# Kernel optimization log

Measured on AMD Instinct MI355X. Metric: run time of the kernel, lower is better.

## Reference

```python
import jax, jax.numpy as jnp
import numpy as np

L_IN, L_FREQ, L_OUT = 128, 64, 64
C_IN, C_OUT, T_DIM = 64, 64, 256
SPIN = 1

# ---------- self-contained spin-weighted SHT (MW sampling), replacing s2fft ----------

def _mw_thetas(L, extended):
    n = 2 * L - 1 if extended else L
    return (2 * np.arange(n) + 1) * np.pi / (2 * L - 1)

def _wigner_d_stack(L, thetas, n):
    # d^l_{m,n}(theta) = <l,m| exp(-i theta Jy) |l,n>, computed via eigh of the
    # Hermitian angular-momentum operator Jy. Output (ntheta, L, 2L-1), m at col L-1+m.
    nth = len(thetas)
    out = np.zeros((nth, L, 2 * L - 1), dtype=np.float64)
    for l in range(abs(n), L):
        dim = 2 * l + 1
        m = np.arange(-l, l).astype(np.float64)
        ap = np.sqrt(l * (l + 1.0) - m * (m + 1.0))
        Jy = np.zeros((dim, dim), dtype=np.complex128)
        i = np.arange(dim - 1)
        Jy[i + 1, i] = -0.5j * ap
        Jy[i, i + 1] = 0.5j * ap
        lam, V = np.linalg.eigh(Jy)
        coeff = V * np.conj(V[l + n, :])[None, :]
        phases = np.exp(-1j * np.outer(lam, thetas))
        out[:, l, L - 1 - l:L + l] = (coeff @ phases).T.real
    return out

def _mw_quad_weights(L):
    # per-theta weights on the mirror-extended grid: q_t = (1/(2L-1)) sum_k w(k) e^{ik theta_t}
    # with w(k) = int_0^pi e^{ik t} sin(t) dt
    k = np.arange(-(L - 1), L)
    den = np.where(np.abs(k) == 1, 1, 1 - k * k).astype(np.float64)
    w = np.where(k % 2 == 0, 2.0 / den, 0.0).astype(np.complex128)
    w[k == 1] = 0.5j * np.pi
    w[k == -1] = -0.5j * np.pi
    th = _mw_thetas(L, True)
    return ((w[None, :] * np.exp(1j * np.outer(th, k))).sum(1) / (2 * L - 1)).real

# transform kernels are constants (built once at import, numpy)
_D_FWD = jnp.asarray(_wigner_d_stack(L_IN, _mw_thetas(L_IN, True), -SPIN) * _mw_quad_weights(L_IN)[:, None, None], jnp.float32)
_D_INV = jnp.asarray(_wigner_d_stack(L_OUT, _mw_thetas(L_OUT, False), -SPIN), jnp.float32)
_CL_IN = jnp.asarray(((-1.0) ** SPIN) * np.sqrt((2 * np.arange(L_IN) + 1) / (4 * np.pi)), jnp.float32)
_CL_OUT = jnp.asarray(((-1.0) ** SPIN) * np.sqrt((2 * np.arange(L_OUT) + 1) / (4 * np.pi)), jnp.float32)
_m_all = np.arange(-(L_IN - 1), L_IN)
_PARITY = jnp.asarray(np.where((_m_all + SPIN) % 2 == 0, 1.0, -1.0), jnp.float32)

def sht_forward(x):
    # x: (L_IN, 2*L_IN-1, C) real spatial -> flm: (L_IN, 2*L_IN-1, C) complex, m at L_IN-1+m
    nphi = 2 * L_IN - 1
    ftm = jnp.fft.fftshift(jnp.fft.fft(x, axis=1), axes=1) * (2 * jnp.pi / nphi)
    # mirror extension in theta with (-1)^(m+spin) parity (all channels at once)
    g_ext = jnp.concatenate([ftm, _PARITY[None, :, None] * ftm[::-1][1:]], axis=0)
    flm = jnp.einsum('tlm,tmc->lmc', _D_FWD, g_ext)
    return flm * _CL_IN[:, None, None]

def sht_inverse(flm):
    # flm: (L_OUT, 2*L_OUT-1, C) complex -> (L_OUT, 2*L_OUT-1, C) real spatial
    ftm = jnp.einsum('tlm,lmc->tmc', _D_INV, flm * _CL_OUT[:, None, None])
    return (jnp.fft.ifft(jnp.fft.ifftshift(ftm, axes=1), axis=1) * (2 * L_OUT - 1)).real

def resize_flm(flm, l_in, l_out):
    # centered truncation / zero-pad of (L, 2L-1, C) harmonic coefficients
    if l_out <= l_in:
        d = l_in - l_out
        return flm[:l_out, d:d + 2 * l_out - 1]
    d = l_out - l_in
    return jnp.pad(flm, ((0, d), (d, d), (0, 0)))

# ---------- inputs and parameters ----------

def setup_inputs():
    key = jax.random.key(0)
    ks = jax.random.split(key, 12)
    n = lambda i, shape, s: jax.random.normal(ks[i], shape, jnp.float32) * s
    return {
        'x': jax.random.normal(ks[0], (L_IN, 2 * L_IN - 1, C_IN), jnp.float32),
        't_emb': jax.random.normal(ks[1], (T_DIM,), jnp.float32),
        'spec_conv_w': n(2, (C_IN, C_OUT), (1.0 / C_IN) ** 0.5),
        'spec_conv_b': jnp.zeros((C_OUT,), jnp.float32),
        'spec_wr': n(3, (L_FREQ, C_IN, C_OUT), (0.5 / C_IN) ** 0.5),
        'spec_wi': n(4, (L_FREQ, C_IN, C_OUT), (0.5 / C_IN) ** 0.5),
        'spec_tr_w': n(5, (T_DIM, L_FREQ), (1.0 / T_DIM) ** 0.5),
        'spec_tr_b': jnp.zeros((L_FREQ,), jnp.float32),
        'spec_ti_w': n(6, (T_DIM, L_FREQ), (1.0 / T_DIM) ** 0.5),
        'spec_ti_b': jnp.zeros((L_FREQ,), jnp.float32),
        'spat_conv1_w': n(7, (C_IN, C_OUT), (1.0 / C_IN) ** 0.5),
        'spat_conv1_b': jnp.zeros((C_OUT,), jnp.float32),
        'spat_t_w': n(8, (T_DIM, 2 * C_OUT), (1.0 / T_DIM) ** 0.5),
        'spat_t_b': jnp.zeros((2 * C_OUT,), jnp.float32),
        'spat_weight': n(9, (C_OUT, C_OUT), 0.01),
        'spat_conv2_w': n(10, (C_OUT, C_OUT), (1.0 / C_OUT) ** 0.5),
        'spat_conv2_b': jnp.zeros((C_OUT,), jnp.float32),
        'ln_scale': jnp.ones((C_OUT,), jnp.float32),
        'ln_bias': jnp.zeros((C_OUT,), jnp.float32),
    }

def reference(x, t_emb, spec_conv_w, spec_conv_b, spec_wr, spec_wi, spec_tr_w, spec_tr_b, spec_ti_w, spec_ti_b, spat_conv1_w, spat_conv1_b, spat_t_w, spat_t_b, spat_weight, spat_conv2_w, spat_conv2_b, ln_scale, ln_bias):
    # ----- SphericalSpectralTimeConv branch -----
    flm = sht_forward(x)                                   # (L_IN, 2L_IN-1, C_IN) complex
    flm = resize_flm(flm, L_IN, L_FREQ)                    # (L_FREQ, 2L_FREQ-1, C_IN)
    conv_flm = jnp.einsum('lmi,io->lmo', flm, spec_conv_w) + spec_conv_b
    t_c = (t_emb @ spec_tr_w + spec_tr_b) + 1j * (t_emb @ spec_ti_w + spec_ti_b)   # (L_FREQ,)
    w = t_c[:, None, None] * (spec_wr + 1j * spec_wi)      # (L_FREQ, C_IN, C_OUT)
    flm = jnp.einsum('lmi,lio->lmo', flm, w) + conv_flm
    xs = sht_inverse(resize_flm(flm, L_FREQ, L_OUT))       # (L_OUT, 2L_OUT-1, C_OUT) real
    xs = xs / (jnp.linalg.norm(xs, axis=-1, keepdims=True) + 1e-6)
    # ----- SpatialTimeConv branch (path='down') -----
    h = jnp.einsum('lmi,io->lmo', x, spat_conv1_w) + spat_conv1_b
    t = t_emb @ spat_t_w + spat_t_b
    w_t, b_t = t[:C_OUT], t[C_OUT:]
    h = jnp.einsum('lmi,io->lmo', h, w_t[None, :] * spat_weight)
    h = sht_inverse(resize_flm(sht_forward(h), L_IN, L_OUT))
    h = jnp.einsum('lmi,io->lmo', h, spat_conv2_w) + spat_conv2_b + b_t
    # ----- combine: add, gelu, LayerNorm (eps=1e-6 over channels) -----
    y = jax.nn.gelu(xs + h)
    mu = jnp.mean(y, axis=-1, keepdims=True)
    var = jnp.var(y, axis=-1, keepdims=True)
    return (y - mu) * jax.lax.rsqrt(var + 1e-6) * ln_scale + ln_bias
```

## Files before the change

### kernel.cpp

```cpp
#include <hip/hip_runtime.h>
#include <math.h>

#define DPI 3.141592653589793238462643383279502884

__device__ float g_Deff[1040384];
__device__ float g_Dinv[520192];
__device__ int g_wig_done = 0;

__device__ __forceinline__ float wave_sum64(float v) {
#pragma unroll
  for (int off = 32; off > 0; off >>= 1) v += __shfl_xor(v, off, 64);
  return v;
}

__device__ __forceinline__ float gelu_tanh(float v) {
  float u = 0.7978845608028654f * (v + 0.044715f * v * v * v);
  return 0.5f * v * (1.0f + tanhf(u));
}

#define CN255F ((float)(-2.0 * DPI / 255.0))
#define CN127F ((float)(2.0 * DPI / 127.0))

__device__ __forceinline__ void dft_block(int idx, int tid, const float* __restrict__ x,
                                          float* __restrict__ Are, float* __restrict__ Aim,
                                          float* __restrict__ Bre, float* __restrict__ Bim,
                                          char* sm) {
  float* xs_ = (float*)sm;
  int t = idx >> 2, ph = (idx >> 1) & 1, mh = idx & 1;
  float* ore = ph ? Bre : Are;
  float* oim = ph ? Bim : Aim;
  int pbase = ph * 128;
  int Ktot = ph ? 127 : 128;
  int cg_ = tid & 15, mg = tid >> 4;
  float wr[2], wi[2], rc[2], rs[2];
#pragma unroll
  for (int j = 0; j < 2; ++j) {
    int m = mh * 32 + mg * 2 + j;
    __sincosf(CN255F * (float)m, &rs[j], &rc[j]);
    int r0 = (m * pbase) % 255;
    __sincosf(CN255F * (float)r0, &wi[j], &wr[j]);
  }
  float accr[2][4], acci[2][4];
#pragma unroll
  for (int j = 0; j < 2; ++j)
#pragma unroll
    for (int q = 0; q < 4; ++q) { accr[j][q] = 0.f; acci[j][q] = 0.f; }
  for (int k0 = 0; k0 < Ktot; k0 += 64) {
    int kn = (Ktot - k0 < 64) ? Ktot - k0 : 64;
    __syncthreads();
    {
      const float4* src = (const float4*)(x + ((size_t)t * 255 + pbase + k0) * 64);
      float4* dst = (float4*)xs_;
      int lim = kn * 16;
#pragma unroll
      for (int q = 0; q < 4; ++q) {
        int fidx = tid + q * 256;
        if (fidx < lim) dst[fidx] = src[fidx];
      }
    }
    __syncthreads();
#pragma unroll 2
    for (int k = 0; k < kn; ++k) {
      float4 xv = *(const float4*)&xs_[k * 64 + cg_ * 4];
      float xv4[4] = {xv.x, xv.y, xv.z, xv.w};
#pragma unroll
      for (int j = 0; j < 2; ++j) {
#pragma unroll
        for (int q = 0; q < 4; ++q) {
          accr[j][q] = fmaf(xv4[q], wr[j], accr[j][q]);
          acci[j][q] = fmaf(xv4[q], wi[j], acci[j][q]);
        }
        float nw = wr[j] * rc[j] - wi[j] * rs[j];
        wi[j] = fmaf(wr[j], rs[j], wi[j] * rc[j]);
        wr[j] = nw;
      }
    }
  }
#pragma unroll
  for (int j = 0; j < 2; ++j) {
    int mi = mh * 32 + mg * 2 + j;
    size_t ob = ((size_t)t * 64 + mi) * 64 + cg_ * 4;
    *(float4*)(ore + ob) = make_float4(accr[j][0], accr[j][1], accr[j][2], accr[j][3]);
    *(float4*)(oim + ob) = make_float4(acci[j][0], acci[j][1], acci[j][2], acci[j][3]);
  }
}

__device__ __forceinline__ void wigner_block(int wb, int tid, char* sm) {
  if (__hip_atomic_load(&g_wig_done, __ATOMIC_RELAXED, __HIP_MEMORY_SCOPE_AGENT)) return;
  float* LF = (float*)sm;
  double* red = (double*)(sm + 512);
  float* clf = (float*)(sm + 1024);
  int mode = (wb < 128) ? 0 : 1;
  int t, mm;
  if (mode == 0) { t = wb; mm = tid; }
  else { mm = wb - 128; t = (tid < 64) ? tid : 63; }
  if (tid < 64) clf[tid] = (float)(-sqrt((2.0 * tid + 1.0) / (4.0 * DPI)));
  if (tid < 128) LF[tid] = (tid == 0) ? 0.f : logf((float)tid);
  __syncthreads();
  for (int s = 1; s < 128; s <<= 1) {
    float add = (tid < 128 && tid >= s) ? LF[tid - s] : 0.f;
    __syncthreads();
    if (tid < 128) LF[tid] += add;
    __syncthreads();
  }
  double denomN = (mode == 0) ? 255.0 : 127.0;
  double beta = (2.0 * t + 1.0) * DPI / denomN;
  float coeff = 1.0f;
  if (mode == 0) {
    if (tid < 63) {
      int k = 2 * (tid + 1);
      red[tid] = 8.0 * cos((double)k * beta) / (1.0 - (double)k * (double)k);
    } else if (tid == 63) {
      red[63] = 4.0;
    }
    __syncthreads();
    for (int s = 32; s > 0; s >>= 1) {
      if (tid < s) red[tid] += red[tid + s];
      __syncthreads();
    }
    double s = red[0] / 255.0;
    if (t == 127) s *= 0.5;
    coeff = (float)(s * (2.0 * DPI / 255.0));
  }
  bool active = (mode == 0) ? (tid < 127) : (tid < 64);
  if (!active) return;
  int m = mm - 63;
  double chd, shd;
  sincos(0.5 * beta, &shd, &chd);
  float cbf = (float)cos(beta);
  float chf = (float)chd, shf = (float)shd;
  int am = (m < 0) ? -m : m;
  int l0v = (am > 1) ? am : 1;
  float seed;
  if (m == 0) {
    seed = -1.4142135623730951f * shf * chf;
  } else {
    int j = am;
    float lch = logf(chf), lsh = logf(shf);
    float e0 = 0.5f * (LF[2 * j] - LF[j - 1] - LF[j + 1]);
    float expo = (m >= 1) ? e0 + (float)(j - 1) * lch + (float)(j + 1) * lsh
                          : e0 + (float)(j + 1) * lch + (float)(j - 1) * lsh;
    float sv = __expf(expo);
    seed = (m >= 1 && ((m + 1) & 1)) ? -sv : sv;
  }
  float dl = seed, dm1 = 0.0f, S_cur = 0.0f;
  float mf = (float)m;
  for (int l = 0; l < 64; ++l) {
    float val = 0.0f;
    if (l >= l0v) {
      val = dl * coeff * clf[l];
      float Ld = (float)l, lp = Ld + 1.0f;
      float S_next = sqrtf((lp * lp - mf * mf) * (lp * lp - 1.0f));
      float num1 = (2.0f * Ld + 1.0f) * (Ld * lp * cbf + mf);
      float dn = (num1 * dl - lp * S_cur * dm1) / (Ld * S_next);
      dm1 = dl; dl = dn; S_cur = S_next;
    }
    if (mode == 0) g_Deff[((size_t)t * 127 + mm) * 64 + l] = val;
    else g_Dinv[((size_t)mm * 64 + l) * 64 + t] = val;
  }
}

__device__ __forceinline__ void a2_block(int l, int tid, const float* __restrict__ temb,
                                         const float* __restrict__ trw, const float* __restrict__ trb,
                                         const float* __restrict__ tiw, const float* __restrict__ tib,
                                         const float* __restrict__ scw, const float* __restrict__ swr,
                                         const float* __restrict__ swi, float2* __restrict__ A2,
                                         char* sm) {
  float* fb1 = (float*)sm;
  float* fb2 = (float*)(sm + 1024);
  fb1[tid] = temb[tid] * trw[tid * 64 + l];
  fb2[tid] = temb[tid] * tiw[tid * 64 + l];
  __syncthreads();
  for (int s = 128; s > 0; s >>= 1) {
    if (tid < s) { fb1[tid] += fb1[tid + s]; fb2[tid] += fb2[tid + s]; }
    __syncthreads();
  }
  float tr = fb1[0] + trb[l], ti = fb2[0] + tib[l];
  int o = tid & 63, iq = tid >> 6;
#pragma unroll 4
  for (int i = iq * 16; i < iq * 16 + 16; ++i) {
    int idx = (l * 64 + i) * 64 + o;
    float r = swr[idx], s2 = swi[idx];
    A2[idx] = make_float2(scw[i * 64 + o] + tr * r - ti * s2, tr * s2 + ti * r);
  }
}

__device__ __forceinline__ void mstv_block(int tid, const float* __restrict__ temb,
                                           const float* __restrict__ stw, const float* __restrict__ stb,
                                           const float* __restrict__ c1w, const float* __restrict__ c1b,
                                           const float* __restrict__ sweight,
                                           float* __restrict__ tv, float* __restrict__ Mm,
                                           float* __restrict__ bias2, char* sm) {
  float* temb_s = (float*)sm;
  float* swt = (float*)(sm + 1024);
  float* c1s = (float*)(sm + 17408);
  float* tvo_s = (float*)(sm + 34048);
  if (tid < 64) ((float4*)temb_s)[tid] = ((const float4*)temb)[tid];
  for (int q = tid; q < 1024; q += 256) ((float4*)swt)[q] = ((const float4*)sweight)[q];
  for (int e = tid; e < 4096; e += 256) c1s[(e >> 6) * 65 + (e & 63)] = c1w[e];
  __syncthreads();
  if (tid < 128) {
    float a0 = 0.f, a1 = 0.f, a2 = 0.f, a3 = 0.f;
#pragma unroll 8
    for (int k = 0; k < 256; k += 4) {
      a0 = fmaf(temb_s[k],     stw[k * 128 + tid],       a0);
      a1 = fmaf(temb_s[k + 1], stw[(k + 1) * 128 + tid], a1);
      a2 = fmaf(temb_s[k + 2], stw[(k + 2) * 128 + tid], a2);
      a3 = fmaf(temb_s[k + 3], stw[(k + 3) * 128 + tid], a3);
    }
    float tvv = a0 + a1 + a2 + a3 + stb[tid];
    tv[tid] = tvv;
    if (tid < 64) tvo_s[tid] = tvv;
  }
  __syncthreads();
  {
    int j = tid >> 2, ob = (tid & 3) * 16;
    float acc[16];
#pragma unroll
    for (int q = 0; q < 16; ++q) acc[q] = 0.f;
    for (int i = 0; i < 64; ++i) {
      float c = c1s[j * 65 + i];
#pragma unroll
      for (int q = 0; q < 16; ++q) acc[q] = fmaf(c, swt[i * 64 + ob + q], acc[q]);
    }
#pragma unroll
    for (int q = 0; q < 16; ++q) Mm[j * 64 + ob + q] = tvo_s[ob + q] * acc[q];
  }
  if (tid < 64) {
    float acc = 0.f;
#pragma unroll 4
    for (int i = 0; i < 64; ++i) acc = fmaf(c1b[i], swt[i * 64 + tid], acc);
    bias2[tid] = tvo_s[tid] * acc;
  }
}

__global__ __launch_bounds__(256, 2) void ct_pre(
    const float* __restrict__ x,
    float* __restrict__ ftmA_re, float* __restrict__ ftmA_im,
    float* __restrict__ ftmB_re, float* __restrict__ ftmB_im) {
  __shared__ __align__(16) char sm[16384];
  int vb = blockIdx.x;
  int tid = threadIdx.x;
  if (vb < 255) wigner_block(vb, tid, sm);
  else dft_block(vb - 255, tid, x, ftmA_re, ftmA_im, ftmB_re, ftmB_im, sm);
}

__global__ __launch_bounds__(256) void ct_projf(const float* __restrict__ fAre,
                                                const float* __restrict__ fAim,
                                                const float* __restrict__ fBre,
                                                const float* __restrict__ fBim,
                                                float* __restrict__ flmA_re, float* __restrict__ flmA_im,
                                                float* __restrict__ flmB_re, float* __restrict__ flmB_im,
                                                const float* __restrict__ temb,
                                                const float* __restrict__ trw, const float* __restrict__ trb,
                                                const float* __restrict__ tiw, const float* __restrict__ tib,
                                                const float* __restrict__ scw, const float* __restrict__ swr,
                                                const float* __restrict__ swi, float2* __restrict__ A2,
                                                const float* __restrict__ stw, const float* __restrict__ stb,
                                                const float* __restrict__ c1w, const float* __restrict__ c1b,
                                                const float* __restrict__ sweight,
                                                float* __restrict__ tv, float* __restrict__ Mm,
                                                float* __restrict__ bias2) {
  __shared__ __align__(16) char sm[40960];
  int tile = blockIdx.x;
  int tid = threadIdx.x;
  if (tile >= 508) {
    if (tile < 572) a2_block(tile - 508, tid, temb, trw, trb, tiw, tib, scw, swr, swi, A2, sm);
    else mstv_block(tid, temb, stw, stb, c1w, c1b, sweight, tv, Mm, bias2, sm);
    return;
  }
  float (*Dsh)[32] = (float(*)[32])(sm);
  float (*fr_)[64] = (float(*)[64])(sm + 8192);
  float (*fi_)[64] = (float(*)[64])(sm + 24576);
  int mm = tile >> 2, lh = (tile >> 1) & 1, th = tile & 1;
  float* ore = th ? flmB_re : flmA_re;
  float* oim = th ? flmB_im : flmA_im;
  int tb = th * 64;
  int mi = (mm >= 63) ? (mm - 63) : (63 - mm);
  float csign = (mm >= 63) ? 1.0f : -1.0f;
  int cg_ = tid & 15, lg = tid >> 4;
  for (int e = tid; e < 64 * 32; e += 256) {
    int r = e >> 5, li = e & 31;
    Dsh[r][li] = g_Deff[((size_t)(tb + r) * 127 + mm) * 64 + lh * 32 + li];
  }
  for (int e = tid; e < 64 * 64; e += 256) {
    int r = e >> 6, c = e & 63;
    size_t idx = ((size_t)(tb + r) * 64 + mi) * 64 + c;
    fr_[r][c] = fAre[idx] + fBre[idx];
    fi_[r][c] = csign * (fAim[idx] + fBim[idx]);
  }
  __syncthreads();
  float ar[2][4], ai[2][4];
#pragma unroll
  for (int li = 0; li < 2; ++li)
#pragma unroll
    for (int q = 0; q < 4; ++q) { ar[li][q] = 0.f; ai[li][q] = 0.f; }
#pragma unroll 4
  for (int k = 0; k < 64; ++k) {
    float4 fr4 = *(const float4*)&fr_[k][cg_ * 4];
    float4 fi4 = *(const float4*)&fi_[k][cg_ * 4];
    float2 d2 = *(const float2*)&Dsh[k][lg * 2];
    float frv[4] = {fr4.x, fr4.y, fr4.z, fr4.w};
    float fiv[4] = {fi4.x, fi4.y, fi4.z, fi4.w};
    float dv[2] = {d2.x, d2.y};
#pragma unroll
    for (int li = 0; li < 2; ++li)
#pragma unroll
      for (int q = 0; q < 4; ++q) {
        ar[li][q] = fmaf(dv[li], frv[q], ar[li][q]);
        ai[li][q] = fmaf(dv[li], fiv[q], ai[li][q]);
      }
  }
#pragma unroll
  for (int li = 0; li < 2; ++li) {
    size_t row = ((size_t)mm * 64 + lh * 32 + lg * 2 + li) * 64 + cg_ * 4;
    *(float4*)(ore + row) = make_float4(ar[li][0], ar[li][1], ar[li][2], ar[li][3]);
    *(float4*)(oim + row) = make_float4(ai[li][0], ai[li][1], ai[li][2], ai[li][3]);
  }
}

__global__ __launch_bounds__(256) void ct_mix(const float* __restrict__ flmA_re,
                                              const float* __restrict__ flmA_im,
                                              const float* __restrict__ flmB_re,
                                              const float* __restrict__ flmB_im,
                                              const float2* __restrict__ A2,
                                              const float* __restrict__ Mm,
                                              const float* __restrict__ scb,
                                              const float* __restrict__ bias2,
                                              float* __restrict__ s_re, float* __restrict__ s_im,
                                              float* __restrict__ h_re, float* __restrict__ h_im) {
  __shared__ float Ar_[64][32], Ai_[64][32], Msh[64][32];
  __shared__ float Br_[64][65], Bi_[64][65];
  __shared__ float rb[256];
  int l = blockIdx.x, mh = blockIdx.y, oh = blockIdx.z;
  int tid = threadIdx.x;
  int og = tid & 15, mg = tid >> 4;
  rb[tid] = (mh == 0 && tid < 128) ? g_Deff[((size_t)tid * 127 + 63) * 64 + l] : 0.f;
  __syncthreads();
  for (int s = 128; s > 0; s >>= 1) {
    if (tid < s) rb[tid] += rb[tid + s];
    __syncthreads();
  }
  float slv = rb[0];
  for (int e = tid; e < 64 * 32; e += 256) {
    int r = e >> 5, oi = e & 31;
    float2 aa = A2[((size_t)l * 64 + r) * 64 + oh * 32 + oi];
    Ar_[r][oi] = aa.x; Ai_[r][oi] = aa.y;
    Msh[r][oi] = Mm[r * 64 + oh * 32 + oi];
  }
  for (int e = tid; e < 64 * 64; e += 256) {
    int mi = e >> 6, i = e & 63;
    int gmm = mh * 64 + mi; if (gmm > 126) gmm = 126;
    size_t idx = ((size_t)gmm * 64 + l) * 64 + i;
    Br_[mi][i] = flmA_re[idx] + flmB_re[idx];
    Bi_[mi][i] = flmA_im[idx] + flmB_im[idx];
  }
  __syncthreads();
  int o0 = oh * 32 + og * 2;
  float b0[2] = {scb[o0], scb[o0 + 1]};
  float sr[4][2], si[4][2], hr[4][2], hi[4][2];
#pragma unroll
  for (int jm = 0; jm < 4; ++jm)
#pragma unroll
    for (int qo = 0; qo < 2; ++qo) {
      sr[jm][qo] = b0[qo]; si[jm][qo] = 0.f; hr[jm][qo] = 0.f; hi[jm][qo] = 0.f;
    }
#pragma unroll 4
  for (int k = 0; k < 64; ++k) {
    float2 ar2 = *(const float2*)&Ar_[k][og * 2];
    float2 ai2 = *(const float2*)&Ai_[k][og * 2];
    float2 mv2 = *(const float2*)&Msh[k][og * 2];
    float br4[4], bi4[4];
#pragma unroll
    for (int jm = 0; jm < 4; ++jm) {
      br4[jm] = Br_[mg * 4 + jm][k];
      bi4[jm] = Bi_[mg * 4 + jm][k];
    }
    float arv[2] = {ar2.x, ar2.y}, aiv[2] = {ai2.x, ai2.y}, mvv[2] = {mv2.x, mv2.y};
#pragma unroll
    for (int jm = 0; jm < 4; ++jm)
#pragma unroll
      for (int qo = 0; qo < 2; ++qo) {
        sr[jm][qo] = fmaf(br4[jm], arv[qo], sr[jm][qo]);
        sr[jm][qo] = fmaf(-bi4[jm], aiv[qo], sr[jm][qo]);
        si[jm][qo] = fmaf(br4[jm], aiv[qo], si[jm][qo]);
        si[jm][qo] = fmaf(bi4[jm], arv[qo], si[jm][qo]);
        hr[jm][qo] = fmaf(br4[jm], mvv[qo], hr[jm][qo]);
        hi[jm][qo] = fmaf(bi4[jm], mvv[qo], hi[jm][qo]);
      }
  }
  float bb[2] = {bias2[o0], bias2[o0 + 1]};
#pragma unroll
  for (int jm = 0; jm < 4; ++jm) {
    int gmm = mh * 64 + mg * 4 + jm;
    if (gmm > 126) continue;
    if (gmm == 63) {
#pragma unroll
      for (int qo = 0; qo < 2; ++qo)
        hr[jm][qo] = fmaf(255.0f * slv, bb[qo], hr[jm][qo]);
    }
    size_t row = ((size_t)gmm * 64 + l) * 64 + o0;
    *(float2*)(s_re + row) = make_float2(sr[jm][0], sr[jm][1]);
    *(float2*)(s_im + row) = make_float2(si[jm][0], si[jm][1]);
    *(float2*)(h_re + row) = make_float2(hr[jm][0], hr[jm][1]);
    *(float2*)(h_im + row) = make_float2(hi[jm][0], hi[jm][1]);
  }
}

__global__ __launch_bounds__(256) void ct_proji(const float* __restrict__ s_re,
                                                const float* __restrict__ s_im,
                                                const float* __restrict__ h_re,
                                                const float* __restrict__ h_im,
                                                float* __restrict__ fos_re, float* __restrict__ fos_im,
                                                float* __restrict__ foh_re, float* __restrict__ foh_im) {
  __shared__ float Dsh[64][64];
  __shared__ float Br_[64][32], Bi_[64][32];
  int mm = blockIdx.x, br = blockIdx.y, ch = blockIdx.z;
  const float* ire = br ? h_re : s_re;
  const float* iim = br ? h_im : s_im;
  float* ore = br ? foh_re : fos_re;
  float* oim = br ? foh_im : fos_im;
  int tid = threadIdx.x;
  int cg_ = tid & 15, tg = tid >> 4;
  for (int e = tid; e < 64 * 64; e += 256) {
    int r = e >> 6, tt = e & 63;
    Dsh[r][tt] = g_Dinv[((size_t)mm * 64 + r) * 64 + tt];
  }
  for (int e = tid; e < 64 * 32; e += 256) {
    int r = e >> 5, cc = e & 31;
    size_t idx = ((size_t)mm * 64 + r) * 64 + ch * 32 + cc;
    Br_[r][cc] = ire[idx];
    Bi_[r][cc] = iim[idx];
  }
  __syncthreads();
  float ar[4][2], ai[4][2];
#pragma unroll
  for (int j = 0; j < 4; ++j)
#pragma unroll
    for (int q = 0; q < 2; ++q) { ar[j][q] = 0.f; ai[j][q] = 0.f; }
#pragma unroll 4
  for (int k = 0; k < 64; ++k) {
    float4 d4 = *(const float4*)&Dsh[k][tg * 4];
    float2 fr2 = *(const float2*)&Br_[k][cg_ * 2];
    float2 fi2 = *(const float2*)&Bi_[k][cg_ * 2];
    float dv[4] = {d4.x, d4.y, d4.z, d4.w};
    float frv[2] = {fr2.x, fr2.y}, fiv[2] = {fi2.x, fi2.y};
#pragma unroll
    for (int j = 0; j < 4; ++j)
#pragma unroll
      for (int q = 0; q < 2; ++q) {
        ar[j][q] = fmaf(dv[j], frv[q], ar[j][q]);
        ai[j][q] = fmaf(dv[j], fiv[q], ai[j][q]);
      }
  }
#pragma unroll
  for (int j = 0; j < 4; ++j) {
    int t = tg * 4 + j;
    size_t ob = ((size_t)t * 127 + mm) * 64 + ch * 32 + cg_ * 2;
    *(float2*)(ore + ob) = make_float2(ar[j][0], ar[j][1]);
    *(float2*)(oim + ob) = make_float2(ai[j][0], ai[j][1]);
  }
}

__global__ __launch_bounds__(256) void ct_idft(const float* __restrict__ fos_re,
                                               const float* __restrict__ fos_im,
                                               const float* __restrict__ foh_re,
                                               const float* __restrict__ foh_im,
                                               float* __restrict__ xsbA, float* __restrict__ xsbB,
                                               float* __restrict__ hsbA, float* __restrict__ hsbB) {
  __shared__ float Br_[32][64], Bi_[32][64];
  int t = blockIdx.x, br = blockIdx.y;
  int z = blockIdx.z;
  int ph = z >> 1, kh = z & 1;
  const float* fre = br ? foh_re : fos_re;
  const float* fim = br ? foh_im : fos_im;
  float* outp = br ? (kh ? hsbB : hsbA) : (kh ? xsbB : xsbA);
  int kbase = kh * 64;
  int Ktot = kh ? 63 : 64;
  int tid = threadIdx.x;
  int cg_ = tid & 15, pg = tid >> 4;
  float wc[4], ws[4], rc[4], rs[4];
#pragma unroll
  for (int j = 0; j < 4; ++j) {
    int gp = ph * 64 + pg * 4 + j; if (gp > 126) gp = 126;
    __sincosf(CN127F * (float)gp, &rs[j], &rc[j]);
    int r0 = ((kbase - 63) * gp) % 127;
    __sincosf(CN127F * (float)r0, &ws[j], &wc[j]);
  }
  float acc[4][4];
#pragma unroll
  for (int j = 0; j < 4; ++j)
#pragma unroll
    for (int q = 0; q < 4; ++q) acc[j][q] = 0.f;
  for (int k0 = 0; k0 < Ktot; k0 += 32) {
    int kn = (Ktot - k0 < 32) ? Ktot - k0 : 32;
    __syncthreads();
    for (int e = tid; e < 32 * 64; e += 256) {
      int r = e >> 6, j = e & 63;
      if (r < kn) {
        size_t bidx = ((size_t)t * 127 + kbase + k0 + r) * 64 + j;
        Br_[r][j] = fre[bidx]; Bi_[r][j] = fim[bidx];
      }
    }
    __syncthreads();
#pragma unroll 2
    for (int k = 0; k < kn; ++k) {
      float4 b_r = *(const float4*)&Br_[k][cg_ * 4];
      float4 b_i = *(const float4*)&Bi_[k][cg_ * 4];
      float brv[4] = {b_r.x, b_r.y, b_r.z, b_r.w};
      float biv[4] = {b_i.x, b_i.y, b_i.z, b_i.w};
#pragma unroll
      for (int j = 0; j < 4; ++j) {
#pragma unroll
        for (int q = 0; q < 4; ++q) {
          acc[j][q] = fmaf(brv[q], wc[j], acc[j][q]);
          acc[j][q] = fmaf(biv[q], -ws[j], acc[j][q]);
        }
        float nw = wc[j] * rc[j] - ws[j] * rs[j];
        ws[j] = fmaf(wc[j], rs[j], ws[j] * rc[j]);
        wc[j] = nw;
      }
    }
  }
#pragma unroll
  for (int j = 0; j < 4; ++j) {
    int gp = ph * 64 + pg * 4 + j;
    if (gp > 126) continue;
    *(float4*)(outp + ((size_t)t * 127 + gp) * 64 + cg_ * 4) =
        make_float4(acc[j][0], acc[j][1], acc[j][2], acc[j][3]);
  }
}

__global__ __launch_bounds__(256) void ct_fin(const float* __restrict__ xsbA,
                                              const float* __restrict__ xsbB,
                                              const float* __restrict__ hsbA,
                                              const float* __restrict__ hsbB,
                                              const float* __restrict__ c2w,
                                              const float* __restrict__ c2b,
                                              const float* __restrict__ tv,
                                              const float* __restrict__ lns,
                                              const float* __restrict__ lnb,
                                              float* __restrict__ out) {
  int w = threadIdx.x >> 6, lane = threadIdx.x & 63;
  size_t row = (size_t)blockIdx.x * 4 + w;
  size_t base = row * 64 + lane;
  float hv = hsbA[base] + hsbB[base];
  float xv = xsbA[base] + xsbB[base];
  float acc = c2b[lane] + tv[64 + lane];
#pragma unroll 16
  for (int i = 0; i < 64; ++i)
    acc = fmaf(__shfl(hv, i, 64), c2w[i * 64 + lane], acc);
  float ss = wave_sum64(xv * xv);
  xv = xv / (sqrtf(ss) + 1e-6f);
  float y = xv + acc;
  float g = gelu_tanh(y);
  float mu = wave_sum64(g) * (1.0f / 64.0f);
  float d = g - mu;
  float var = wave_sum64(d * d) * (1.0f / 64.0f);
  out[base] = d * rsqrtf(var + 1e-6f) * lns[lane] + lnb[lane];
  if (blockIdx.x == 0 && threadIdx.x == 0)
    __hip_atomic_store(&g_wig_done, 1, __ATOMIC_RELAXED, __HIP_MEMORY_SCOPE_AGENT);
}

extern "C" void kernel_launch(void* const* d_in, const int* in_sizes, int n_in,
                              void* d_out, int out_size, void* d_ws, size_t ws_size,
                              hipStream_t stream) {
  const float* x = (const float*)d_in[0];
  const float* temb = (const float*)d_in[1];
  const float* scw = (const float*)d_in[2];
  const float* scb = (const float*)d_in[3];
  const float* swr = (const float*)d_in[4];
  const float* swi = (const float*)d_in[5];
  const float* strw = (const float*)d_in[6];
  const float* strb = (const float*)d_in[7];
  const float* stiw = (const float*)d_in[8];
  const float* stib = (const float*)d_in[9];
  const float* c1w = (const float*)d_in[10];
  const float* c1b = (const float*)d_in[11];
  const float* stw = (const float*)d_in[12];
  const float* stb = (const float*)d_in[13];
  const float* sweight = (const float*)d_in[14];
  const float* c2w = (const float*)d_in[15];
  const float* c2b = (const float*)d_in[16];
  const float* lns = (const float*)d_in[17];
  const float* lnb = (const float*)d_in[18];
  float* out = (float*)d_out;

  char* base = (char*)d_ws;
  size_t off = 0;
  auto alloc = [&](size_t bytes) -> void* {
    void* p = base + off;
    off += (bytes + 255) & ~(size_t)255;
    return p;
  };
  float* tv = (float*)alloc(128 * sizeof(float));
  float* Mm = (float*)alloc(4096 * sizeof(float));
  float* bias2 = (float*)alloc(64 * sizeof(float));
  float2* A2 = (float2*)alloc(262144 * sizeof(float2));
  float* fosbuf = (float*)alloc(1040384 * sizeof(float));
  float* ftmA_re = (float*)alloc(524288 * sizeof(float));
  float* ftmA_im = (float*)alloc(524288 * sizeof(float));
  float* ftmB_re = (float*)alloc(524288 * sizeof(float));
  float* ftmB_im = (float*)alloc(524288 * sizeof(float));
  float* flmA_re = (float*)alloc(520192 * sizeof(float));
  float* flmA_im = (float*)alloc(520192 * sizeof(float));
  float* flmB_re = (float*)alloc(520192 * sizeof(float));
  float* flmB_im = (float*)alloc(520192 * sizeof(float));
  if (off > ws_size) return;
  float* s_re = ftmA_re;
  float* s_im = ftmA_im;
  float* h_re = ftmB_re;
  float* h_im = ftmB_im;
  float* fos_re = fosbuf;
  float* fos_im = fosbuf + 520192;
  float* foh_re = flmA_re;
  float* foh_im = flmA_im;
  float* xsbA = flmB_re;
  float* xsbB = flmB_im;
  float* hsbA = ftmA_re;
  float* hsbB = ftmA_im;

  hipLaunchKernelGGL(ct_pre, dim3(767), dim3(256), 0, stream,
                     x, ftmA_re, ftmA_im, ftmB_re, ftmB_im);
  hipLaunchKernelGGL(ct_projf, dim3(573), dim3(256), 0, stream,
                     ftmA_re, ftmA_im, ftmB_re, ftmB_im,
                     flmA_re, flmA_im, flmB_re, flmB_im,
                     temb, strw, strb, stiw, stib, scw, swr, swi, A2,
                     stw, stb, c1w, c1b, sweight, tv, Mm, bias2);
  hipLaunchKernelGGL(ct_mix, dim3(64, 2, 2), dim3(256), 0, stream,
                     flmA_re, flmA_im, flmB_re, flmB_im, A2, Mm, scb, bias2,
                     s_re, s_im, h_re, h_im);
  hipLaunchKernelGGL(ct_proji, dim3(127, 2, 2), dim3(256), 0, stream,
                     s_re, s_im, h_re, h_im, fos_re, fos_im, foh_re, foh_im);
  hipLaunchKernelGGL(ct_idft, dim3(64, 2, 4), dim3(256), 0, stream,
                     fos_re, fos_im, foh_re, foh_im, xsbA, xsbB, hsbA, hsbB);
  hipLaunchKernelGGL(ct_fin, dim3(2032), dim3(256), 0, stream, xsbA, xsbB, hsbA, hsbB,
                     c2w, c2b, tv, lns, lnb, out);
}
```

Before: 179.0 us.

## Fuse forward projection, spectral mix and inverse projection into one per-m kernel

The forward Wigner projection, the channel mixing and the inverse Wigner projection are merged into a single ct_mid kernel with one block per (m, output-half). Intermediate flm and mixed spectra stay in shared memory instead of going through global buffers. The A2 and Mm/bias precomputation moves into ct_pre, leaving four launches instead of six. The trade-off is only 254 blocks, heavier per-block work and large shared memory use. The forward projection is also computed twice, once for each output half.

Result: no change. 182.2 us (+1.8%).

```diff
diff --git a/kernel.cpp b/kernel.cpp
--- a/kernel.cpp
+++ b/kernel.cpp
@@ -235,230 +235,182 @@
 }
 
 __global__ __launch_bounds__(256, 2) void ct_pre(
-    const float* __restrict__ x,
+    const float* __restrict__ x, const float* __restrict__ temb,
+    const float* __restrict__ trw, const float* __restrict__ trb,
+    const float* __restrict__ tiw, const float* __restrict__ tib,
+    const float* __restrict__ stw, const float* __restrict__ stb,
+    const float* __restrict__ scw, const float* __restrict__ swr,
+    const float* __restrict__ swi, const float* __restrict__ c1w,
+    const float* __restrict__ c1b, const float* __restrict__ sweight,
+    float2* __restrict__ A2, float* __restrict__ Mm,
+    float* __restrict__ bias2, float* __restrict__ tv,
     float* __restrict__ ftmA_re, float* __restrict__ ftmA_im,
     float* __restrict__ ftmB_re, float* __restrict__ ftmB_im) {
-  __shared__ __align__(16) char sm[16384];
+  __shared__ __align__(16) char sm[34304];
   int vb = blockIdx.x;
   int tid = threadIdx.x;
   if (vb < 255) wigner_block(vb, tid, sm);
-  else dft_block(vb - 255, tid, x, ftmA_re, ftmA_im, ftmB_re, ftmB_im, sm);
-}
-
-__global__ __launch_bounds__(256) void ct_projf(const float* __restrict__ fAre,
-                                                const float* __restrict__ fAim,
-                                                const float* __restrict__ fBre,
-                                                const float* __restrict__ fBim,
-                                                float* __restrict__ flmA_re, float* __restrict__ flmA_im,
-                                                float* __restrict__ flmB_re, float* __restrict__ flmB_im,
-                                                const float* __restrict__ temb,
-                                                const float* __restrict__ trw, const float* __restrict__ trb,
-                                                const float* __restrict__ tiw, const float* __restrict__ tib,
-                                                const float* __restrict__ scw, const float* __restrict__ swr,
-                                                const float* __restrict__ swi, float2* __restrict__ A2,
-                                                const float* __restrict__ stw, const float* __restrict__ stb,
-                                                const float* __restrict__ c1w, const float* __restrict__ c1b,
-                                                const float* __restrict__ sweight,
-                                                float* __restrict__ tv, float* __restrict__ Mm,
-                                                float* __restrict__ bias2) {
-  __shared__ __align__(16) char sm[40960];
-  int tile = blockIdx.x;
+  else if (vb < 767) dft_block(vb - 255, tid, x, ftmA_re, ftmA_im, ftmB_re, ftmB_im, sm);
+  else if (vb < 831) a2_block(vb - 767, tid, temb, trw, trb, tiw, tib, scw, swr, swi, A2, sm);
+  else mstv_block(tid, temb, stw, stb, c1w, c1b, sweight, tv, Mm, bias2, sm);
+}
+
+__global__ __launch_bounds__(256, 2) void ct_mid(
+    const float* __restrict__ fAre, const float* __restrict__ fAim,
+    const float* __restrict__ fBre, const float* __restrict__ fBim,
+    const float2* __restrict__ A2, const float* __restrict__ Mm,
+    const float* __restrict__ scb, const float* __restrict__ bias2,
+    float* __restrict__ fos_re, float* __restrict__ fos_im,
+    float* __restrict__ foh_re, float* __restrict__ foh_im) {
+  __shared__ __align__(16) char sm[69888];
+  int mm = blockIdx.x, oh = blockIdx.y;
   int tid = threadIdx.x;
-  if (tile >= 508) {
-    if (tile < 572) a2_block(tile - 508, tid, temb, trw, trb, tiw, tib, scw, swr, swi, A2, sm);
-    else mstv_block(tid, temb, stw, stb, c1w, c1b, sweight, tv, Mm, bias2, sm);
-    return;
-  }
-  float (*Dsh)[32] = (float(*)[32])(sm);
-  float (*fr_)[64] = (float(*)[64])(sm + 8192);
-  float (*fi_)[64] = (float(*)[64])(sm + 24576);
-  int mm = tile >> 2, lh = (tile >> 1) & 1, th = tile & 1;
-  float* ore = th ? flmB_re : flmA_re;
-  float* oim = th ? flmB_im : flmA_im;
-  int tb = th * 64;
   int mi = (mm >= 63) ? (mm - 63) : (63 - mm);
   float csign = (mm >= 63) ? 1.0f : -1.0f;
-  int cg_ = tid & 15, lg = tid >> 4;
-  for (int e = tid; e < 64 * 32; e += 256) {
-    int r = e >> 5, li = e & 31;
-    Dsh[r][li] = g_Deff[((size_t)(tb + r) * 127 + mm) * 64 + lh * 32 + li];
-  }
-  for (int e = tid; e < 64 * 64; e += 256) {
-    int r = e >> 6, c = e & 63;
-    size_t idx = ((size_t)(tb + r) * 64 + mi) * 64 + c;
-    fr_[r][c] = fAre[idx] + fBre[idx];
-    fi_[r][c] = csign * (fAim[idx] + fBim[idx]);
-  }
-  __syncthreads();
-  float ar[2][4], ai[2][4];
-#pragma unroll
-  for (int li = 0; li < 2; ++li)
+
+  float* flm_re = (float*)(sm);
+  float* flm_im = (float*)(sm + 17408);
+  float* sS_re  = (float*)(sm + 34816);
+  float* sS_im  = (float*)(sm + 43520);
+  float* hS_re  = (float*)(sm + 52224);
+  float* hS_im  = (float*)(sm + 60928);
+  float* slS    = (float*)(sm + 69632);
+  float* fre_s = (float*)(sm + 34816);
+  float* fim_s = (float*)(sm + 43008);
+  float* Dt    = (float*)(sm + 51200);
+  float* Dsh = (float*)(sm);
+
+  int cg = tid & 15, lg = tid >> 4;
+  float ar[4][4], ai[4][4], sl4[4];
+#pragma unroll
+  for (int li = 0; li < 4; ++li) {
+    sl4[li] = 0.f;
 #pragma unroll
     for (int q = 0; q < 4; ++q) { ar[li][q] = 0.f; ai[li][q] = 0.f; }
+  }
+  for (int t0 = 0; t0 < 128; t0 += 32) {
+    __syncthreads();
+    for (int e = tid; e < 2048; e += 256) {
+      int r = e >> 6, c = e & 63;
+      size_t idx = ((size_t)(t0 + r) * 64 + mi) * 64 + c;
+      fre_s[r * 64 + c] = fAre[idx] + fBre[idx];
+      fim_s[r * 64 + c] = csign * (fAim[idx] + fBim[idx]);
+      Dt[r * 64 + c] = g_Deff[((size_t)(t0 + r) * 127 + mm) * 64 + c];
+    }
+    __syncthreads();
+#pragma unroll 2
+    for (int k = 0; k < 32; ++k) {
+      float4 fr4 = *(const float4*)&fre_s[k * 64 + cg * 4];
+      float4 fi4 = *(const float4*)&fim_s[k * 64 + cg * 4];
+      float4 d4 = *(const float4*)&Dt[k * 64 + lg * 4];
+      float frv[4] = {fr4.x, fr4.y, fr4.z, fr4.w};
+      float fiv[4] = {fi4.x, fi4.y, fi4.z, fi4.w};
+      float dv[4] = {d4.x, d4.y, d4.z, d4.w};
+#pragma unroll
+      for (int li = 0; li < 4; ++li) {
+        sl4[li] += dv[li];
+#pragma unroll
+        for (int q = 0; q < 4; ++q) {
+          ar[li][q] = fmaf(dv[li], frv[q], ar[li][q]);
+          ai[li][q] = fmaf(dv[li], fiv[q], ai[li][q]);
+        }
+      }
+    }
+  }
+  __syncthreads();
+#pragma unroll
+  for (int li = 0; li < 4; ++li) {
+    int l = lg * 4 + li;
+    *(float4*)&flm_re[l * 68 + cg * 4] = make_float4(ar[li][0], ar[li][1], ar[li][2], ar[li][3]);
+    *(float4*)&flm_im[l * 68 + cg * 4] = make_float4(ai[li][0], ai[li][1], ai[li][2], ai[li][3]);
+    if (cg == 0) slS[l] = sl4[li];
+  }
+  __syncthreads();
+
+  {
+    int lB = tid >> 2;
+    int oq = tid & 3;
+    int o0 = oh * 32 + oq * 8;
+    float sr[8], si2[8], hr[8], hi2[8];
+#pragma unroll
+    for (int q = 0; q < 8; ++q) {
+      sr[q] = scb[o0 + q]; si2[q] = 0.f; hr[q] = 0.f; hi2[q] = 0.f;
+    }
+    for (int i = 0; i < 64; ++i) {
+      float fr = flm_re[lB * 68 + i];
+      float fi = flm_im[lB * 68 + i];
+      const float2* a2p = &A2[((size_t)lB * 64 + i) * 64 + o0];
+      const float* mmp = &Mm[i * 64 + o0];
+#pragma unroll
+      for (int q = 0; q < 8; ++q) {
+        float2 a = a2p[q];
+        float mv = mmp[q];
+        sr[q] = fmaf(fr, a.x, fmaf(-fi, a.y, sr[q]));
+        si2[q] = fmaf(fr, a.y, fmaf(fi, a.x, si2[q]));
+        hr[q] = fmaf(fr, mv, hr[q]);
+        hi2[q] = fmaf(fi, mv, hi2[q]);
+      }
+    }
+    if (mm == 63) {
+      float sl = 255.0f * slS[lB];
+#pragma unroll
+      for (int q = 0; q < 8; ++q) hr[q] = fmaf(sl, bias2[o0 + q], hr[q]);
+    }
+    int ob = oq * 8;
+#pragma unroll
+    for (int q = 0; q < 8; ++q) {
+      sS_re[lB * 34 + ob + q] = sr[q];
+      sS_im[lB * 34 + ob + q] = si2[q];
+      hS_re[lB * 34 + ob + q] = hr[q];
+      hS_im[lB * 34 + ob + q] = hi2[q];
+    }
+  }
+  __syncthreads();
+
+  for (int e = tid; e < 4096; e += 256) {
+    int r = e >> 6, tt = e & 63;
+    Dsh[r * 64 + tt] = g_Dinv[((size_t)mm * 64 + r) * 64 + tt];
+  }
+  __syncthreads();
+  {
+    int cg2 = tid & 15, tg = tid >> 4;
+    float as_r[4][2], as_i[4][2], ah_r[4][2], ah_i[4][2];
+#pragma unroll
+    for (int j = 0; j < 4; ++j)
+#pragma unroll
+      for (int q = 0; q < 2; ++q) {
+        as_r[j][q] = 0.f; as_i[j][q] = 0.f; ah_r[j][q] = 0.f; ah_i[j][q] = 0.f;
+      }
 #pragma unroll 4
-  for (int k = 0; k < 64; ++k) {
-    float4 fr4 = *(const float4*)&fr_[k][cg_ * 4];
-    float4 fi4 = *(const float4*)&fi_[k][cg_ * 4];
-    float2 d2 = *(const float2*)&Dsh[k][lg * 2];
-    float frv[4] = {fr4.x, fr4.y, fr4.z, fr4.w};
-    float fiv[4] = {fi4.x, fi4.y, fi4.z, fi4.w};
-    float dv[2] = {d2.x, d2.y};
-#pragma unroll
-    for (int li = 0; li < 2; ++li)
-#pragma unroll
-      for (int q = 0; q < 4; ++q) {
-        ar[li][q] = fmaf(dv[li], frv[q], ar[li][q]);
-        ai[li][q] = fmaf(dv[li], fiv[q], ai[li][q]);
-      }
-  }
-#pragma unroll
-  for (int li = 0; li < 2; ++li) {
-    size_t row = ((size_t)mm * 64 + lh * 32 + lg * 2 + li) * 64 + cg_ * 4;
-    *(float4*)(ore + row) = make_float4(ar[li][0], ar[li][1], ar[li][2], ar[li][3]);
-    *(float4*)(oim + row) = make_float4(ai[li][0], ai[li][1], ai[li][2], ai[li][3]);
-  }
-}
-
-__global__ __launch_bounds__(256) void ct_mix(const float* __restrict__ flmA_re,
-                                              const float* __restrict__ flmA_im,
-                                              const float* __restrict__ flmB_re,
-                                              const float* __restrict__ flmB_im,
-                                              const float2* __restrict__ A2,
-                                              const float* __restrict__ Mm,
-                                              const float* __restrict__ scb,
-                                              const float* __restrict__ bias2,
-                                              float* __restrict__ s_re, float* __restrict__ s_im,
-                                              float* __restrict__ h_re, float* __restrict__ h_im) {
-  __shared__ float Ar_[64][32], Ai_[64][32], Msh[64][32];
-  __shared__ float Br_[64][65], Bi_[64][65];
-  __shared__ float rb[256];
-  int l = blockIdx.x, mh = blockIdx.y, oh = blockIdx.z;
-  int tid = threadIdx.x;
-  int og = tid & 15, mg = tid >> 4;
-  rb[tid] = (mh == 0 && tid < 128) ? g_Deff[((size_t)tid * 127 + 63) * 64 + l] : 0.f;
-  __syncthreads();
-  for (int s = 128; s > 0; s >>= 1) {
-    if (tid < s) rb[tid] += rb[tid + s];
-    __syncthreads();
-  }
-  float slv = rb[0];
-  for (int e = tid; e < 64 * 32; e += 256) {
-    int r = e >> 5, oi = e & 31;
-    float2 aa = A2[((size_t)l * 64 + r) * 64 + oh * 32 + oi];
-    Ar_[r][oi] = aa.x; Ai_[r][oi] = aa.y;
-    Msh[r][oi] = Mm[r * 64 + oh * 32 + oi];
-  }
-  for (int e = tid; e < 64 * 64; e += 256) {
-    int mi = e >> 6, i = e & 63;
-    int gmm = mh * 64 + mi; if (gmm > 126) gmm = 126;
-    size_t idx = ((size_t)gmm * 64 + l) * 64 + i;
-    Br_[mi][i] = flmA_re[idx] + flmB_re[idx];
-    Bi_[mi][i] = flmA_im[idx] + flmB_im[idx];
-  }
-  __syncthreads();
-  int o0 = oh * 32 + og * 2;
-  float b0[2] = {scb[o0], scb[o0 + 1]};
-  float sr[4][2], si[4][2], hr[4][2], hi[4][2];
-#pragma unroll
-  for (int jm = 0; jm < 4; ++jm)
-#pragma unroll
-    for (int qo = 0; qo < 2; ++qo) {
-      sr[jm][qo] = b0[qo]; si[jm][qo] = 0.f; hr[jm][qo] = 0.f; hi[jm][qo] = 0.f;
-    }
-#pragma unroll 4
-  for (int k = 0; k < 64; ++k) {
-    float2 ar2 = *(const float2*)&Ar_[k][og * 2];
-    float2 ai2 = *(const float2*)&Ai_[k][og * 2];
-    float2 mv2 = *(const float2*)&Msh[k][og * 2];
-    float br4[4], bi4[4];
-#pragma unroll
-    for (int jm = 0; jm < 4; ++jm) {
-      br4[jm] = Br_[mg * 4 + jm][k];
-      bi4[jm] = Bi_[mg * 4 + jm][k];
-    }
-    float arv[2] = {ar2.x, ar2.y}, aiv[2] = {ai2.x, ai2.y}, mvv[2] = {mv2.x, mv2.y};
-#pragma unroll
-    for (int jm = 0; jm < 4; ++jm)
-#pragma unroll
-      for (int qo = 0; qo < 2; ++qo) {
-        sr[jm][qo] = fmaf(br4[jm], arv[qo], sr[jm][qo]);
-        sr[jm][qo] = fmaf(-bi4[jm], aiv[qo], sr[jm][qo]);
-        si[jm][qo] = fmaf(br4[jm], aiv[qo], si[jm][qo]);
-        si[jm][qo] = fmaf(bi4[jm], arv[qo], si[jm][qo]);
-        hr[jm][qo] = fmaf(br4[jm], mvv[qo], hr[jm][qo]);
-        hi[jm][qo] = fmaf(bi4[jm], mvv[qo], hi[jm][qo]);
-      }
-  }
-  float bb[2] = {bias2[o0], bias2[o0 + 1]};
-#pragma unroll
-  for (int jm = 0; jm < 4; ++jm) {
-    int gmm = mh * 64 + mg * 4 + jm;
-    if (gmm > 126) continue;
-    if (gmm == 63) {
-#pragma unroll
-      for (int qo = 0; qo < 2; ++qo)
-        hr[jm][qo] = fmaf(255.0f * slv, bb[qo], hr[jm][qo]);
-    }
-    size_t row = ((size_t)gmm * 64 + l) * 64 + o0;
-    *(float2*)(s_re + row) = make_float2(sr[jm][0], sr[jm][1]);
-    *(float2*)(s_im + row) = make_float2(si[jm][0], si[jm][1]);
-    *(float2*)(h_re + row) = make_float2(hr[jm][0], hr[jm][1]);
-    *(float2*)(h_im + row) = make_float2(hi[jm][0], hi[jm][1]);
-  }
-}
-
-__global__ __launch_bounds__(256) void ct_proji(const float* __restrict__ s_re,
-                                                const float* __restrict__ s_im,
-                                                const float* __restrict__ h_re,
-                                                const float* __restrict__ h_im,
-                                                float* __restrict__ fos_re, float* __restrict__ fos_im,
-                                                float* __restrict__ foh_re, float* __restrict__ foh_im) {
-  __shared__ float Dsh[64][64];
-  __shared__ float Br_[64][32], Bi_[64][32];
-  int mm = blockIdx.x, br = blockIdx.y, ch = blockIdx.z;
-  const float* ire = br ? h_re : s_re;
-  const float* iim = br ? h_im : s_im;
-  float* ore = br ? foh_re : fos_re;
-  float* oim = br ? foh_im : fos_im;
-  int tid = threadIdx.x;
-  int cg_ = tid & 15, tg = tid >> 4;
-  for (int e = tid; e < 64 * 64; e += 256) {
-    int r = e >> 6, tt = e & 63;
-    Dsh[r][tt] = g_Dinv[((size_t)mm * 64 + r) * 64 + tt];
-  }
-  for (int e = tid; e < 64 * 32; e += 256) {
-    int r = e >> 5, cc = e & 31;
-    size_t idx = ((size_t)mm * 64 + r) * 64 + ch * 32 + cc;
-    Br_[r][cc] = ire[idx];
-    Bi_[r][cc] = iim[idx];
-  }
-  __syncthreads();
-  float ar[4][2], ai[4][2];
-#pragma unroll
-  for (int j = 0; j < 4; ++j)
-#pragma unroll
-    for (int q = 0; q < 2; ++q) { ar[j][q] = 0.f; ai[j][q] = 0.f; }
-#pragma unroll 4
-  for (int k = 0; k < 64; ++k) {
-    float4 d4 = *(const float4*)&Dsh[k][tg * 4];
-    float2 fr2 = *(const float2*)&Br_[k][cg_ * 2];
-    float2 fi2 = *(const float2*)&Bi_[k][cg_ * 2];
-    float dv[4] = {d4.x, d4.y, d4.z, d4.w};
-    float frv[2] = {fr2.x, fr2.y}, fiv[2] = {fi2.x, fi2.y};
-#pragma unroll
-    for (int j = 0; j < 4; ++j)
-#pragma unroll
-      for (int q = 0; q < 2; ++q) {
-        ar[j][q] = fmaf(dv[j], frv[q], ar[j][q]);
-        ai[j][q] = fmaf(dv[j], fiv[q], ai[j][q]);
-      }
-  }
-#pragma unroll
-  for (int j = 0; j < 4; ++j) {
-    int t = tg * 4 + j;
-    size_t ob = ((size_t)t * 127 + mm) * 64 + ch * 32 + cg_ * 2;
-    *(float2*)(ore + ob) = make_float2(ar[j][0], ar[j][1]);
-    *(float2*)(oim + ob) = make_float2(ai[j][0], ai[j][1]);
+    for (int l = 0; l < 64; ++l) {
+      float4 d4 = *(const float4*)&Dsh[l * 64 + tg * 4];
+      float2 s_r = *(const float2*)&sS_re[l * 34 + cg2 * 2];
+      float2 s_i = *(const float2*)&sS_im[l * 34 + cg2 * 2];
+      float2 h_r = *(const float2*)&hS_re[l * 34 + cg2 * 2];
+      float2 h_i = *(const float2*)&hS_im[l * 34 + cg2 * 2];
+      float dv[4] = {d4.x, d4.y, d4.z, d4.w};
+      float srv[2] = {s_r.x, s_r.y}, siv[2] = {s_i.x, s_i.y};
+      float hrv[2] = {h_r.x, h_r.y}, hiv[2] = {h_i.x, h_i.y};
+#pragma unroll
+      for (int j = 0; j < 4; ++j)
+#pragma unroll
+        for (int q = 0; q < 2; ++q) {
+          as_r[j][q] = fmaf(dv[j], srv[q], as_r[j][q]);
+          as_i[j][q] = fmaf(dv[j], siv[q], as_i[j][q]);
+          ah_r[j][q] = fmaf(dv[j], hrv[q], ah_r[j][q]);
+          ah_i[j][q] = fmaf(dv[j], hiv[q], ah_i[j][q]);
+        }
+    }
+    int c0 = oh * 32 + cg2 * 2;
+#pragma unroll
+    for (int j = 0; j < 4; ++j) {
+      int t = tg * 4 + j;
+      size_t ob = ((size_t)t * 127 + mm) * 64 + c0;
+      *(float2*)(fos_re + ob) = make_float2(as_r[j][0], as_r[j][1]);
+      *(float2*)(fos_im + ob) = make_float2(as_i[j][0], as_i[j][1]);
+      *(float2*)(foh_re + ob) = make_float2(ah_r[j][0], ah_r[j][1]);
+      *(float2*)(foh_im + ob) = make_float2(ah_i[j][0], ah_i[j][1]);
+    }
   }
 }
 
@@ -597,41 +549,29 @@
   float* Mm = (float*)alloc(4096 * sizeof(float));
   float* bias2 = (float*)alloc(64 * sizeof(float));
   float2* A2 = (float2*)alloc(262144 * sizeof(float2));
-  float* fosbuf = (float*)alloc(1040384 * sizeof(float));
+  float* fos_re = (float*)alloc(520192 * sizeof(float));
+  float* fos_im = (float*)alloc(520192 * sizeof(float));
+  float* foh_re = (float*)alloc(520192 * sizeof(float));
+  float* foh_im = (float*)alloc(520192 * sizeof(float));
   float* ftmA_re = (float*)alloc(524288 * sizeof(float));
   float* ftmA_im = (float*)alloc(524288 * sizeof(float));
   float* ftmB_re = (float*)alloc(524288 * sizeof(float));
   float* ftmB_im = (float*)alloc(524288 * sizeof(float));
-  float* flmA_re = (float*)alloc(520192 * sizeof(float));
-  float* flmA_im = (float*)alloc(520192 * sizeof(float));
-  float* flmB_re = (float*)alloc(520192 * sizeof(float));
-  float* flmB_im = (float*)alloc(520192 * sizeof(float));
   if (off > ws_size) return;
-  float* s_re = ftmA_re;
-  float* s_im = ftmA_im;
-  float* h_re = ftmB_re;
-  float* h_im = ftmB_im;
-  float* fos_re = fosbuf;
-  float* fos_im = fosbuf + 520192;
-  float* foh_re = flmA_re;
-  float* foh_im = flmA_im;
-  float* xsbA = flmB_re;
-  float* xsbB = flmB_im;
-  float* hsbA = ftmA_re;
-  float* hsbB = ftmA_im;
-
-  hipLaunchKernelGGL(ct_pre, dim3(767), dim3(256), 0, stream,
-                     x, ftmA_re, ftmA_im, ftmB_re, ftmB_im);
-  hipLaunchKernelGGL(ct_projf, dim3(573), dim3(256), 0, stream,
+  float* xsbA = ftmA_re;
+  float* xsbB = ftmA_im;
+  float* hsbA = ftmB_re;
+  float* hsbB = ftmB_im;
+
+  hipLaunchKernelGGL(ct_pre, dim3(832), dim3(256), 0, stream,
+                     x, temb, strw, strb, stiw, stib, stw, stb,
+                     scw, swr, swi, c1w, c1b, sweight,
+                     A2, Mm, bias2, tv,
+                     ftmA_re, ftmA_im, ftmB_re, ftmB_im);
+  hipLaunchKernelGGL(ct_mid, dim3(127, 2), dim3(256), 0, stream,
                      ftmA_re, ftmA_im, ftmB_re, ftmB_im,
-                     flmA_re, flmA_im, flmB_re, flmB_im,
-                     temb, strw, strb, stiw, stib, scw, swr, swi, A2,
-                     stw, stb, c1w, c1b, sweight, tv, Mm, bias2);
-  hipLaunchKernelGGL(ct_mix, dim3(64, 2, 2), dim3(256), 0, stream,
-                     flmA_re, flmA_im, flmB_re, flmB_im, A2, Mm, scb, bias2,
-                     s_re, s_im, h_re, h_im);
-  hipLaunchKernelGGL(ct_proji, dim3(127, 2, 2), dim3(256), 0, stream,
-                     s_re, s_im, h_re, h_im, fos_re, fos_im, foh_re, foh_im);
+                     A2, Mm, scb, bias2,
+                     fos_re, fos_im, foh_re, foh_im);
   hipLaunchKernelGGL(ct_idft, dim3(64, 2, 4), dim3(256), 0, stream,
                      fos_re, fos_im, foh_re, foh_im, xsbA, xsbB, hsbA, hsbB);
   hipLaunchKernelGGL(ct_fin, dim3(2032), dim3(256), 0, stream, xsbA, xsbB, hsbA, hsbB,
```
